# Performance work log

Hardware: AMD Instinct MI355X
Metric: run time of the kernel (lower is better)

## Reference

```python
import jax, jax.numpy as jnp
import numpy as np

N_NODES = 100000
N_EDGES = 1600000
DIM = 128


def setup_inputs() -> dict:
    key = jax.random.key(0)
    k1, k2, k3 = jax.random.split(key, 3)
    src = jax.random.randint(k1, (N_EDGES,), 0, N_NODES, dtype=jnp.int64 if jax.config.jax_enable_x64 else jnp.int32)
    # offset in [1, N) guarantees no self-loops (matches add_remaining_self_loops semantics cleanly)
    off = jax.random.randint(k2, (N_EDGES,), 1, N_NODES, dtype=src.dtype)
    dst = (src + off) % N_NODES
    edges = jnp.stack([src, dst], axis=1)  # [E, 2]
    x = jax.random.normal(k3, (N_NODES, DIM), dtype=jnp.float32)
    weight1 = jnp.ones((1, DIM), dtype=jnp.float32)
    bias1 = jnp.zeros((DIM,), dtype=jnp.float32)
    weight2 = jnp.ones((1, DIM), dtype=jnp.float32)
    bias2 = jnp.zeros((DIM,), dtype=jnp.float32)
    return {"edges": edges, "x": x, "weight1": weight1, "bias1": bias1,
            "weight2": weight2, "bias2": bias2}


def _gcn_norm(src_all, dst_all, num_nodes, dtype):
    # symmetric normalization: deg from row (src), norm_e = d^-1/2[src] * d^-1/2[dst]
    ones = jnp.ones(src_all.shape[0], dtype=dtype)
    deg = jax.ops.segment_sum(ones, src_all, num_segments=num_nodes)
    dinv = jnp.where(deg > 0, deg ** -0.5, 0.0).astype(dtype)
    return dinv[src_all] * dinv[dst_all]


def _gcn_layer(x, src_all, dst_all, norm, weight, bias):
    # GCNAlign_GCNConv: x = x * weight (elementwise, weight [1,D]);
    # out[i] = sum_{e: dst_e = i} norm_e * x[src_e]; then + bias
    x = x * weight
    msgs = norm[:, None] * x[src_all]          # [E+N, D] gather
    out = jax.ops.segment_sum(msgs, dst_all, num_segments=x.shape[0])  # scatter-add
    return out + bias


def reference(edges, x, weight1, bias1, weight2, bias2):
    num_nodes = x.shape[0]
    src, dst = edges[:, 0], edges[:, 1]
    loop = jnp.arange(num_nodes, dtype=src.dtype)
    src_all = jnp.concatenate([src, loop])
    dst_all = jnp.concatenate([dst, loop])
    norm = _gcn_norm(src_all, dst_all, num_nodes, x.dtype)
    # Encoder.forward (gcn-align, feat_drop=0): layer -> relu -> layer
    h = _gcn_layer(x, src_all, dst_all, norm, weight1, bias1)
    h = jax.nn.relu(h)
    h = _gcn_layer(h, src_all, dst_all, norm, weight2, bias2)
    return h
```

## Files before the change

kernel.cpp:

```cpp
#include <hip/hip_runtime.h>

#define DIM 128
#define EPB_A 8192
#define BSH 10
#define BNODES 1024
#define CAPB 18432
#define NBMAX 128

#if __has_builtin(__builtin_amdgcn_cvt_f32_ubyte0)
#define CVTU0 __builtin_amdgcn_cvt_f32_ubyte0
#define CVTU1 __builtin_amdgcn_cvt_f32_ubyte1
#define CVTU2 __builtin_amdgcn_cvt_f32_ubyte2
#define CVTU3 __builtin_amdgcn_cvt_f32_ubyte3
#else
__device__ __forceinline__ float CVTU0(unsigned u) { return (float)(u & 0xffu); }
__device__ __forceinline__ float CVTU1(unsigned u) { return (float)((u >> 8) & 0xffu); }
__device__ __forceinline__ float CVTU2(unsigned u) { return (float)((u >> 16) & 0xffu); }
__device__ __forceinline__ float CVTU3(unsigned u) { return (float)((u >> 24) & 0xffu); }
#endif


__global__ __launch_bounds__(256) void histscat(const int2* __restrict__ edges, int E,
                                                int* __restrict__ bcnt,
                                                int* __restrict__ scnt,
                                                unsigned* __restrict__ ebuck,
                                                unsigned short* __restrict__ sbuck,
                                                int NB) {
    __shared__ int hdst[NBMAX], hsrc[NBMAX], cdst[NBMAX], csrc[NBMAX];
    int tid = threadIdx.x;
    if (tid < NBMAX) { hdst[tid] = 0; hsrc[tid] = 0; }
    __syncthreads();
    int base = blockIdx.x * EPB_A;
    int cnt = min(EPB_A, E - base);
    for (int i = tid; i < cnt; i += 256) {
        int2 ed = edges[base + i];
        atomicAdd(&hdst[ed.y >> BSH], 1);
        atomicAdd(&hsrc[ed.x >> BSH], 1);
    }
    __syncthreads();
    if (tid < NB) {
        if (hdst[tid] > 0) cdst[tid] = atomicAdd(&bcnt[tid], hdst[tid]);
        if (hsrc[tid] > 0) csrc[tid] = atomicAdd(&scnt[tid], hsrc[tid]);
    }
    __syncthreads();
    for (int i = tid; i < cnt; i += 256) {
        int2 ed = edges[base + i];
        int bd = ed.y >> BSH, bs = ed.x >> BSH;
        int p = atomicAdd(&cdst[bd], 1);
        ebuck[(size_t)bd * CAPB + p] = ((unsigned)ed.x << BSH) | (unsigned)(ed.y & (BNODES - 1));
        int q = atomicAdd(&csrc[bs], 1);
        sbuck[(size_t)bs * CAPB + q] = (unsigned short)(ed.x & (BNODES - 1));
    }
}

__global__ __launch_bounds__(256) void passD(const unsigned short* __restrict__ sbuck,
                                             const int* __restrict__ scnt,
                                             float* __restrict__ dinv, int N) {
    __shared__ int cnt[BNODES];
    int b = blockIdx.x, tid = threadIdx.x;
    int m = scnt[b];
    const unsigned short* sb = sbuck + (size_t)b * CAPB;
    for (int k = tid; k < BNODES; k += 256) cnt[k] = 0;
    __syncthreads();
    for (int i = tid; i < m; i += 256) atomicAdd(&cnt[sb[i]], 1);
    __syncthreads();
    int n0 = b << BSH;
    for (int k = tid; k < BNODES; k += 256) {
        int node = n0 + k;
        if (node < N) dinv[node] = rsqrtf((float)(cnt[k] + 1));
    }
}

__global__ void conv_q8(const float4* __restrict__ xin, const float* __restrict__ dinv,
                        uint2* __restrict__ qx, float* __restrict__ scx, int n8) {
    int i = blockIdx.x * blockDim.x + threadIdx.x;
    if (i >= n8) return;
    int node = i >> 4, ln = i & 15;
    float dv = dinv[node];
    float4 v0 = xin[2 * i], v1 = xin[2 * i + 1];
    float y0 = dv * v0.x, y1 = dv * v0.y, y2 = dv * v0.z, y3 = dv * v0.w;
    float y4 = dv * v1.x, y5 = dv * v1.y, y6 = dv * v1.z, y7 = dv * v1.w;
    float mx = fmaxf(fmaxf(fmaxf(fabsf(y0), fabsf(y1)), fmaxf(fabsf(y2), fabsf(y3))),
                     fmaxf(fmaxf(fabsf(y4), fabsf(y5)), fmaxf(fabsf(y6), fabsf(y7))));
    mx = fmaxf(mx, __shfl_xor(mx, 1));
    mx = fmaxf(mx, __shfl_xor(mx, 2));
    mx = fmaxf(mx, __shfl_xor(mx, 4));
    mx = fmaxf(mx, __shfl_xor(mx, 8));
    float inv = (mx > 0.f) ? 127.f / mx : 0.f;
    unsigned q0 = (unsigned)(__float2int_rn(y0 * inv) + 128);
    unsigned q1 = (unsigned)(__float2int_rn(y1 * inv) + 128);
    unsigned q2 = (unsigned)(__float2int_rn(y2 * inv) + 128);
    unsigned q3 = (unsigned)(__float2int_rn(y3 * inv) + 128);
    unsigned q4 = (unsigned)(__float2int_rn(y4 * inv) + 128);
    unsigned q5 = (unsigned)(__float2int_rn(y5 * inv) + 128);
    unsigned q6 = (unsigned)(__float2int_rn(y6 * inv) + 128);
    unsigned q7 = (unsigned)(__float2int_rn(y7 * inv) + 128);
    uint2 ov;
    ov.x = q0 | (q1 << 8) | (q2 << 16) | (q3 << 24);
    ov.y = q4 | (q5 << 8) | (q6 << 16) | (q7 << 24);
    qx[(size_t)node * 16 + ln] = ov;
    if (ln == 0) scx[node] = mx * (1.f / 127.f);
}

__global__ __launch_bounds__(256) void passC(const unsigned* __restrict__ ebuck,
                                             const int* __restrict__ bcnt,
                                             int* __restrict__ rowoff,
                                             int* __restrict__ csr_src,
                                             int N, int E, int NB) {
    __shared__ int cnt[BNODES];
    __shared__ int fill[BNODES];
    __shared__ int psum[256];
    int b = blockIdx.x, tid = threadIdx.x;
    psum[tid] = (tid < NB && tid < b) ? bcnt[tid] : 0;
    __syncthreads();
    for (int off = 128; off > 0; off >>= 1) {
        if (tid < off) psum[tid] += psum[tid + off];
        __syncthreads();
    }
    int eb0 = psum[0];
    int m = bcnt[b];
    __syncthreads();
    const unsigned* eb = ebuck + (size_t)b * CAPB;
    for (int k = tid; k < BNODES; k += 256) cnt[k] = 0;
    __syncthreads();
    for (int i = tid; i < m; i += 256)
        atomicAdd(&cnt[eb[i] & (BNODES - 1u)], 1);
    __syncthreads();
    int n0 = (b << BSH) + 4 * tid;
    int v[4]; int s = 0;
    #pragma unroll
    for (int j = 0; j < 4; ++j) {
        v[j] = (n0 + j < N) ? cnt[4 * tid + j] + 1 : 0;
        s += v[j];
    }
    psum[tid] = s;
    __syncthreads();
    for (int off = 1; off < 256; off <<= 1) {
        int t = (tid >= off) ? psum[tid - off] : 0;
        __syncthreads();
        psum[tid] += t;
        __syncthreads();
    }
    int run = psum[tid] - s;
    int csrb = eb0 + (b << BSH);
    #pragma unroll
    for (int j = 0; j < 4; ++j) {
        int node = n0 + j;
        int idx = 4 * tid + j;
        if (node < N) rowoff[node] = csrb + run;
        fill[idx] = run;
        run += v[j];
    }
    if (b == NB - 1 && tid == 0) rowoff[N] = E + N;
    __syncthreads();
    for (int i = tid; i < m; i += 256) {
        unsigned u = eb[i];
        int p = atomicAdd(&fill[u & (BNODES - 1u)], 1);
        csr_src[csrb + p] = (int)(u >> BSH);
    }
    __syncthreads();
    #pragma unroll
    for (int j = 0; j < 4; ++j) {
        int node = n0 + j;
        int idx = 4 * tid + j;
        if (node < N) csr_src[csrb + fill[idx]] = node;
    }
}


#define ACCQ(r, sc) do {                                                   \
    a0 = fmaf(sc, CVTU0(r.x), a0); a1 = fmaf(sc, CVTU1(r.x), a1);          \
    a2 = fmaf(sc, CVTU2(r.x), a2); a3 = fmaf(sc, CVTU3(r.x), a3);          \
    a4 = fmaf(sc, CVTU0(r.y), a4); a5 = fmaf(sc, CVTU1(r.y), a5);          \
    a6 = fmaf(sc, CVTU2(r.y), a6); a7 = fmaf(sc, CVTU3(r.y), a7);          \
} while (0)

template<int BIASED, int LAST>
__global__ __launch_bounds__(256) void gcn_layer(
    const uint2* __restrict__ qin, const float* __restrict__ scin,
    const int* __restrict__ rowoff, const int* __restrict__ csr_src,
    const float* __restrict__ dinv,
    const float* __restrict__ w, const float* __restrict__ bia,
    void* __restrict__ qout, float* __restrict__ scout, int N) {
    int node = blockIdx.x * 4 + (threadIdx.x >> 6);
    if (node >= N) return;
    int lane = threadIdx.x & 63;
    int h  = lane >> 4;
    int ln = lane & 15;
    int gb = lane & 48;
    int start = rowoff[node], end = rowoff[node + 1];
    float a0=0,a1=0,a2=0,a3=0,a4=0,a5=0,a6=0,a7=0;

    int base = start + h;
    int mm = end - base;
    int m = (mm > 0) ? ((mm + 3) >> 2) : 0;
    int j16 = min(m, 16);

    int  msrc = 0;
    float msc = 0.f;
    if (ln < j16) {
        msrc = csr_src[base + 4 * ln];
        msc  = scin[msrc];
    }

    const char* qbase = (const char*)qin + (ln << 3);

    uint2 rb[16];
    #pragma unroll
    for (int j = 0; j < 16; ++j) {
        if (j < j16) {
            int sj = __shfl(msrc, gb + j);
            rb[j] = *(const uint2*)(qbase + (((unsigned)sj) << 7));
        }
    }
    #pragma unroll
    for (int j = 0; j < 16; ++j) {
        if (j < j16) {
            float sc = __shfl(msc, gb + j);
            ACCQ(rb[j], sc);
        }
    }

    float corr_t = 0.f;
    for (int j = 16; j < m; ++j) {
        int s = csr_src[base + 4 * j];
        float sc = scin[s];
        uint2 c = *(const uint2*)(qbase + (((unsigned)s) << 7));
        ACCQ(c, sc);
        if (BIASED && ln == 0) corr_t += sc;
    }

    a0+=__shfl_xor(a0,16); a1+=__shfl_xor(a1,16); a2+=__shfl_xor(a2,16); a3+=__shfl_xor(a3,16);
    a4+=__shfl_xor(a4,16); a5+=__shfl_xor(a5,16); a6+=__shfl_xor(a6,16); a7+=__shfl_xor(a7,16);
    a0+=__shfl_xor(a0,32); a1+=__shfl_xor(a1,32); a2+=__shfl_xor(a2,32); a3+=__shfl_xor(a3,32);
    a4+=__shfl_xor(a4,32); a5+=__shfl_xor(a5,32); a6+=__shfl_xor(a6,32); a7+=__shfl_xor(a7,32);

    if (BIASED) {
        float cv = msc + corr_t;
        cv += __shfl_xor(cv, 1);  cv += __shfl_xor(cv, 2);
        cv += __shfl_xor(cv, 4);  cv += __shfl_xor(cv, 8);
        cv += __shfl_xor(cv, 16); cv += __shfl_xor(cv, 32);
        float c = 128.f * cv;
        a0 -= c; a1 -= c; a2 -= c; a3 -= c; a4 -= c; a5 -= c; a6 -= c; a7 -= c;
    }

    if (h == 0) {
        float dn = dinv[node];
        float4 w0 = ((const float4*)w)[ln * 2],   w1 = ((const float4*)w)[ln * 2 + 1];
        float4 b0 = ((const float4*)bia)[ln * 2], b1 = ((const float4*)bia)[ln * 2 + 1];
        float o0 = fmaf(a0, dn * w0.x, b0.x), o1 = fmaf(a1, dn * w0.y, b0.y);
        float o2 = fmaf(a2, dn * w0.z, b0.z), o3 = fmaf(a3, dn * w0.w, b0.w);
        float o4 = fmaf(a4, dn * w1.x, b1.x), o5 = fmaf(a5, dn * w1.y, b1.y);
        float o6 = fmaf(a6, dn * w1.z, b1.z), o7 = fmaf(a7, dn * w1.w, b1.w);
        if (!LAST) {
            o0 = dn * fmaxf(o0, 0.f); o1 = dn * fmaxf(o1, 0.f);
            o2 = dn * fmaxf(o2, 0.f); o3 = dn * fmaxf(o3, 0.f);
            o4 = dn * fmaxf(o4, 0.f); o5 = dn * fmaxf(o5, 0.f);
            o6 = dn * fmaxf(o6, 0.f); o7 = dn * fmaxf(o7, 0.f);
            float mx = fmaxf(fmaxf(fmaxf(o0, o1), fmaxf(o2, o3)),
                             fmaxf(fmaxf(o4, o5), fmaxf(o6, o7)));
            mx = fmaxf(mx, __shfl_xor(mx, 1));
            mx = fmaxf(mx, __shfl_xor(mx, 2));
            mx = fmaxf(mx, __shfl_xor(mx, 4));
            mx = fmaxf(mx, __shfl_xor(mx, 8));
            float inv = (mx > 0.f) ? 255.f / mx : 0.f;
            unsigned q0 = (unsigned)__float2int_rn(o0 * inv);
            unsigned q1 = (unsigned)__float2int_rn(o1 * inv);
            unsigned q2 = (unsigned)__float2int_rn(o2 * inv);
            unsigned q3 = (unsigned)__float2int_rn(o3 * inv);
            unsigned q4 = (unsigned)__float2int_rn(o4 * inv);
            unsigned q5 = (unsigned)__float2int_rn(o5 * inv);
            unsigned q6 = (unsigned)__float2int_rn(o6 * inv);
            unsigned q7 = (unsigned)__float2int_rn(o7 * inv);
            uint2 ov;
            ov.x = q0 | (q1 << 8) | (q2 << 16) | (q3 << 24);
            ov.y = q4 | (q5 << 8) | (q6 << 16) | (q7 << 24);
            ((uint2*)qout)[(size_t)node * 16 + ln] = ov;
            if (ln == 0) scout[node] = mx * (1.f / 255.f);
        } else {
            ((float4*)qout)[(size_t)node * 32 + ln * 2]     = make_float4(o0, o1, o2, o3);
            ((float4*)qout)[(size_t)node * 32 + ln * 2 + 1] = make_float4(o4, o5, o6, o7);
        }
    }
}


static inline size_t align256(size_t x) { return (x + 255) & ~(size_t)255; }

extern "C" void kernel_launch(void* const* d_in, const int* in_sizes, int n_in,
                              void* d_out, int out_size, void* d_ws, size_t ws_size,
                              hipStream_t stream) {
    const int2*  edges = (const int2*)d_in[0];
    const float* x     = (const float*)d_in[1];
    const float* w1    = (const float*)d_in[2];
    const float* b1    = (const float*)d_in[3];
    const float* w2    = (const float*)d_in[4];
    const float* b2    = (const float*)d_in[5];
    float* out = (float*)d_out;

    const int E = in_sizes[0] / 2;
    const int N = in_sizes[1] / DIM;
    const int TOT = E + N;
    const int NB   = (N + BNODES - 1) >> BSH;
    const int nblk = (E + EPB_A - 1) / EPB_A;

    char* p = (char*)d_ws;
    int*            bcnt    = (int*)p;
    int*            scnt    = bcnt + NB;
    p += align256((size_t)2 * NB * 4);
    float*          dinv    = (float*)p;           p += align256((size_t)N * 4);
    float*          scX     = (float*)p;           p += align256((size_t)N * 4);
    float*          scH     = (float*)p;           p += align256((size_t)N * 4);
    int*            rowoff  = (int*)p;             p += align256((size_t)(N + 1) * 4);
    unsigned*       ebuck   = (unsigned*)p;        p += align256((size_t)NB * CAPB * 4);
    unsigned short* sbuck   = (unsigned short*)p;  p += align256((size_t)NB * CAPB * 2);
    int*            csr_src = (int*)p;             p += align256((size_t)TOT * 4);
    uint2*          qx      = (uint2*)p;           p += align256((size_t)N * DIM);
    uint2*          qh      = (uint2*)p;           p += align256((size_t)N * DIM);

    const int TPB = 256;
    int n8  = N * DIM / 8;
    int nbC = (n8 + TPB - 1) / TPB;

    hipMemsetAsync(bcnt, 0, (size_t)2 * NB * 4, stream);
    histscat<<<nblk, TPB, 0, stream>>>(edges, E, bcnt, scnt, ebuck, sbuck, NB);
    passD<<<NB, TPB, 0, stream>>>(sbuck, scnt, dinv, N);
    conv_q8<<<nbC, TPB, 0, stream>>>((const float4*)x, dinv, qx, scX, n8);
    passC<<<NB, TPB, 0, stream>>>(ebuck, bcnt, rowoff, csr_src, N, E, NB);

    int nbL = (N + 3) / 4;
    gcn_layer<1, 0><<<nbL, TPB, 0, stream>>>(qx, scX, rowoff, csr_src, dinv,
                                             w1, b1, qh, scH, N);
    gcn_layer<0, 1><<<nbL, TPB, 0, stream>>>(qh, scH, rowoff, csr_src, dinv,
                                             w2, b2, out, nullptr, N);
}
```

Before: 207.4 us.

## Streamline GCN gather with clamped indices and widen CSR-build kernel blocks

The layer kernel drops the per-lane validity branches. It clamps each lane's edge index so the first six gather slots always run, and runs the remaining ten slots only when some node in the wave has more than 24 edges. Lanes past the end of a row contribute a zero scale, which replaces the old 16-entry register prefetch buffer. The CSR construction kernels now use larger blocks: histscat loads its 16 edges per thread into registers once and reuses them for both passes, and passD/passC use one thread per node. The cost is redundant loads for short rows and lower occupancy from the larger blocks.

```diff
diff --git a/kernel.cpp b/kernel.cpp
--- a/kernel.cpp
+++ b/kernel.cpp
@@ -20,7 +20,7 @@
 #endif
 
 
-__global__ __launch_bounds__(256) void histscat(const int2* __restrict__ edges, int E,
+__global__ __launch_bounds__(512) void histscat(const int2* __restrict__ edges, int E,
                                                 int* __restrict__ bcnt,
                                                 int* __restrict__ scnt,
                                                 unsigned* __restrict__ ebuck,
@@ -32,10 +32,18 @@
     __syncthreads();
     int base = blockIdx.x * EPB_A;
     int cnt = min(EPB_A, E - base);
-    for (int i = tid; i < cnt; i += 256) {
-        int2 ed = edges[base + i];
-        atomicAdd(&hdst[ed.y >> BSH], 1);
-        atomicAdd(&hsrc[ed.x >> BSH], 1);
+    int2 ed[16];
+    #pragma unroll
+    for (int i = 0; i < 16; ++i) {
+        int idx = tid + i * 512;
+        ed[i] = (idx < cnt) ? edges[base + idx] : make_int2(-1, -1);
+    }
+    #pragma unroll
+    for (int i = 0; i < 16; ++i) {
+        if (ed[i].x >= 0) {
+            atomicAdd(&hdst[ed[i].y >> BSH], 1);
+            atomicAdd(&hsrc[ed[i].x >> BSH], 1);
+        }
     }
     __syncthreads();
     if (tid < NB) {
@@ -43,32 +51,32 @@
         if (hsrc[tid] > 0) csrc[tid] = atomicAdd(&scnt[tid], hsrc[tid]);
     }
     __syncthreads();
-    for (int i = tid; i < cnt; i += 256) {
-        int2 ed = edges[base + i];
-        int bd = ed.y >> BSH, bs = ed.x >> BSH;
-        int p = atomicAdd(&cdst[bd], 1);
-        ebuck[(size_t)bd * CAPB + p] = ((unsigned)ed.x << BSH) | (unsigned)(ed.y & (BNODES - 1));
-        int q = atomicAdd(&csrc[bs], 1);
-        sbuck[(size_t)bs * CAPB + q] = (unsigned short)(ed.x & (BNODES - 1));
-    }
-}
-
-__global__ __launch_bounds__(256) void passD(const unsigned short* __restrict__ sbuck,
-                                             const int* __restrict__ scnt,
-                                             float* __restrict__ dinv, int N) {
+    #pragma unroll
+    for (int i = 0; i < 16; ++i) {
+        if (ed[i].x >= 0) {
+            int bd = ed[i].y >> BSH, bs = ed[i].x >> BSH;
+            int p = atomicAdd(&cdst[bd], 1);
+            ebuck[(size_t)bd * CAPB + p] =
+                ((unsigned)ed[i].x << BSH) | (unsigned)(ed[i].y & (BNODES - 1));
+            int q = atomicAdd(&csrc[bs], 1);
+            sbuck[(size_t)bs * CAPB + q] = (unsigned short)(ed[i].x & (BNODES - 1));
+        }
+    }
+}
+
+__global__ __launch_bounds__(1024) void passD(const unsigned short* __restrict__ sbuck,
+                                              const int* __restrict__ scnt,
+                                              float* __restrict__ dinv, int N) {
     __shared__ int cnt[BNODES];
     int b = blockIdx.x, tid = threadIdx.x;
     int m = scnt[b];
     const unsigned short* sb = sbuck + (size_t)b * CAPB;
-    for (int k = tid; k < BNODES; k += 256) cnt[k] = 0;
-    __syncthreads();
-    for (int i = tid; i < m; i += 256) atomicAdd(&cnt[sb[i]], 1);
-    __syncthreads();
-    int n0 = b << BSH;
-    for (int k = tid; k < BNODES; k += 256) {
-        int node = n0 + k;
-        if (node < N) dinv[node] = rsqrtf((float)(cnt[k] + 1));
-    }
+    cnt[tid] = 0;
+    __syncthreads();
+    for (int i = tid; i < m; i += 1024) atomicAdd(&cnt[sb[i]], 1);
+    __syncthreads();
+    int node = (b << BSH) + tid;
+    if (node < N) dinv[node] = rsqrtf((float)(cnt[tid] + 1));
 }
 
 __global__ void conv_q8(const float4* __restrict__ xin, const float* __restrict__ dinv,
@@ -102,69 +110,53 @@
     if (ln == 0) scx[node] = mx * (1.f / 127.f);
 }
 
-__global__ __launch_bounds__(256) void passC(const unsigned* __restrict__ ebuck,
-                                             const int* __restrict__ bcnt,
-                                             int* __restrict__ rowoff,
-                                             int* __restrict__ csr_src,
-                                             int N, int E, int NB) {
+__global__ __launch_bounds__(1024) void passC(const unsigned* __restrict__ ebuck,
+                                              const int* __restrict__ bcnt,
+                                              int* __restrict__ rowoff,
+                                              int* __restrict__ csr_src,
+                                              int N, int E, int NB) {
     __shared__ int cnt[BNODES];
     __shared__ int fill[BNODES];
-    __shared__ int psum[256];
+    __shared__ int s[BNODES];
+    __shared__ int red[128];
     int b = blockIdx.x, tid = threadIdx.x;
-    psum[tid] = (tid < NB && tid < b) ? bcnt[tid] : 0;
-    __syncthreads();
-    for (int off = 128; off > 0; off >>= 1) {
-        if (tid < off) psum[tid] += psum[tid + off];
+    if (tid < 128) red[tid] = (tid < NB && tid < b) ? bcnt[tid] : 0;
+    __syncthreads();
+    for (int off = 64; off > 0; off >>= 1) {
+        if (tid < off) red[tid] += red[tid + off];
         __syncthreads();
     }
-    int eb0 = psum[0];
+    int eb0 = red[0];
     int m = bcnt[b];
-    __syncthreads();
     const unsigned* eb = ebuck + (size_t)b * CAPB;
-    for (int k = tid; k < BNODES; k += 256) cnt[k] = 0;
-    __syncthreads();
-    for (int i = tid; i < m; i += 256)
+    cnt[tid] = 0;
+    __syncthreads();
+    for (int i = tid; i < m; i += 1024)
         atomicAdd(&cnt[eb[i] & (BNODES - 1u)], 1);
     __syncthreads();
-    int n0 = (b << BSH) + 4 * tid;
-    int v[4]; int s = 0;
-    #pragma unroll
-    for (int j = 0; j < 4; ++j) {
-        v[j] = (n0 + j < N) ? cnt[4 * tid + j] + 1 : 0;
-        s += v[j];
-    }
-    psum[tid] = s;
-    __syncthreads();
-    for (int off = 1; off < 256; off <<= 1) {
-        int t = (tid >= off) ? psum[tid - off] : 0;
+    int node = (b << BSH) + tid;
+    int val = (node < N) ? cnt[tid] + 1 : 0;
+    s[tid] = val;
+    __syncthreads();
+    for (int off = 1; off < 1024; off <<= 1) {
+        int t = (tid >= off) ? s[tid - off] : 0;
         __syncthreads();
-        psum[tid] += t;
+        s[tid] += t;
         __syncthreads();
     }
-    int run = psum[tid] - s;
+    int excl = s[tid] - val;
     int csrb = eb0 + (b << BSH);
-    #pragma unroll
-    for (int j = 0; j < 4; ++j) {
-        int node = n0 + j;
-        int idx = 4 * tid + j;
-        if (node < N) rowoff[node] = csrb + run;
-        fill[idx] = run;
-        run += v[j];
-    }
+    if (node < N) rowoff[node] = csrb + excl;
+    fill[tid] = excl;
     if (b == NB - 1 && tid == 0) rowoff[N] = E + N;
     __syncthreads();
-    for (int i = tid; i < m; i += 256) {
+    for (int i = tid; i < m; i += 1024) {
         unsigned u = eb[i];
         int p = atomicAdd(&fill[u & (BNODES - 1u)], 1);
         csr_src[csrb + p] = (int)(u >> BSH);
     }
     __syncthreads();
-    #pragma unroll
-    for (int j = 0; j < 4; ++j) {
-        int node = n0 + j;
-        int idx = 4 * tid + j;
-        if (node < N) csr_src[csrb + fill[idx]] = node;
-    }
+    if (node < N) csr_src[csrb + fill[tid]] = node;
 }
 
 
@@ -173,6 +165,13 @@
     a2 = fmaf(sc, CVTU2(r.x), a2); a3 = fmaf(sc, CVTU3(r.x), a3);          \
     a4 = fmaf(sc, CVTU0(r.y), a4); a5 = fmaf(sc, CVTU1(r.y), a5);          \
     a6 = fmaf(sc, CVTU2(r.y), a6); a7 = fmaf(sc, CVTU3(r.y), a7);          \
+} while (0)
+
+#define SLOT(j) do {                                                       \
+    int  sj = __shfl(msrc, gb + (j));                                      \
+    float sc = __shfl(msc, gb + (j));                                      \
+    uint2 r = *(const uint2*)(qbase + (((unsigned)sj) << 7));              \
+    ACCQ(r, sc);                                                           \
 } while (0)
 
 template<int BIASED, int LAST>
@@ -184,48 +183,32 @@
     void* __restrict__ qout, float* __restrict__ scout, int N) {
     int node = blockIdx.x * 4 + (threadIdx.x >> 6);
     if (node >= N) return;
+    node = __builtin_amdgcn_readfirstlane(node);
     int lane = threadIdx.x & 63;
     int h  = lane >> 4;
     int ln = lane & 15;
     int gb = lane & 48;
-    int start = rowoff[node], end = rowoff[node + 1];
+    int start = rowoff[node];
+    int mm = rowoff[node + 1] - start;
     float a0=0,a1=0,a2=0,a3=0,a4=0,a5=0,a6=0,a7=0;
 
-    int base = start + h;
-    int mm = end - base;
-    int m = (mm > 0) ? ((mm + 3) >> 2) : 0;
-    int j16 = min(m, 16);
-
-    int  msrc = 0;
-    float msc = 0.f;
-    if (ln < j16) {
-        msrc = csr_src[base + 4 * ln];
-        msc  = scin[msrc];
-    }
+    int off = h + 4 * ln;
+    int offc = min(off, mm - 1);
+    int  msrc = csr_src[start + offc];
+    float msc = (off < mm) ? scin[msrc] : 0.f;
 
     const char* qbase = (const char*)qin + (ln << 3);
 
-    uint2 rb[16];
-    #pragma unroll
-    for (int j = 0; j < 16; ++j) {
-        if (j < j16) {
-            int sj = __shfl(msrc, gb + j);
-            rb[j] = *(const uint2*)(qbase + (((unsigned)sj) << 7));
-        }
-    }
-    #pragma unroll
-    for (int j = 0; j < 16; ++j) {
-        if (j < j16) {
-            float sc = __shfl(msc, gb + j);
-            ACCQ(rb[j], sc);
-        }
-    }
-
+    SLOT(0); SLOT(1); SLOT(2); SLOT(3); SLOT(4); SLOT(5);
+    if (__any(mm > 24)) {
+        SLOT(6); SLOT(7); SLOT(8); SLOT(9); SLOT(10);
+        SLOT(11); SLOT(12); SLOT(13); SLOT(14); SLOT(15);
+    }
     float corr_t = 0.f;
-    for (int j = 16; j < m; ++j) {
-        int s = csr_src[base + 4 * j];
-        float sc = scin[s];
-        uint2 c = *(const uint2*)(qbase + (((unsigned)s) << 7));
+    for (int o = 64 + h; o < mm; o += 4) {
+        int sx = csr_src[start + o];
+        float sc = scin[sx];
+        uint2 c = *(const uint2*)(qbase + (((unsigned)sx) << 7));
         ACCQ(c, sc);
         if (BIASED && ln == 0) corr_t += sc;
     }
@@ -323,10 +306,10 @@
     int nbC = (n8 + TPB - 1) / TPB;
 
     hipMemsetAsync(bcnt, 0, (size_t)2 * NB * 4, stream);
-    histscat<<<nblk, TPB, 0, stream>>>(edges, E, bcnt, scnt, ebuck, sbuck, NB);
-    passD<<<NB, TPB, 0, stream>>>(sbuck, scnt, dinv, N);
+    histscat<<<nblk, 512, 0, stream>>>(edges, E, bcnt, scnt, ebuck, sbuck, NB);
+    passD<<<NB, 1024, 0, stream>>>(sbuck, scnt, dinv, N);
     conv_q8<<<nbC, TPB, 0, stream>>>((const float4*)x, dinv, qx, scX, n8);
-    passC<<<NB, TPB, 0, stream>>>(ebuck, bcnt, rowoff, csr_src, N, E, NB);
+    passC<<<NB, 1024, 0, stream>>>(ebuck, bcnt, rowoff, csr_src, N, E, NB);
 
     int nbL = (N + 3) / 4;
     gcn_layer<1, 0><<<nbL, TPB, 0, stream>>>(qx, scX, rowoff, csr_src, dinv,
```

Result: faster. 166.5 us (-19.7%).
